# Kernel tuning notes

Measured on AMD Instinct MI355X. Metric: run time of the kernel, lower is better.

## Reference

```python
import jax, jax.numpy as jnp
import numpy as np

B, S, HID = 2, 2048, 2048
H = 16
HD = HID // H            # 128
HD2 = HD // 2            # 64 (rope dim per head)
LAT = HID // 8           # 256 latent dim
BASE = 10000.0


def _rotary_table(seq_len):
    # inv_freq over rope dim HD2
    inv_freq = 1.0 / (BASE ** (jnp.arange(0, HD2, 2, dtype=jnp.float32) / HD2))  # [HD2//2]
    pos = jnp.arange(seq_len, dtype=jnp.float32)
    sincos = pos[:, None] * inv_freq[None, :]                 # [S, HD2//2]
    return jnp.concatenate([jnp.sin(sincos), jnp.cos(sincos)], axis=-1)  # [S, HD2]


def _apply_rope(x, emb):
    # x: [B, S, H, HD2]; emb: [S, HD2]
    half = HD2 // 2
    x1, x2 = x[..., :half], x[..., half:]
    sin = emb[None, :, None, :half]
    cos = emb[None, :, None, half:]
    return jnp.concatenate([x1 * cos - x2 * sin, x1 * sin + x2 * cos], axis=-1)


def setup_inputs() -> dict:
    key = jax.random.key(0)
    ks = jax.random.split(key, 9)
    s = 0.02
    return {
        "hidden_states": jax.random.normal(ks[0], (B, S, HID), jnp.float32),
        "w_kv_d": jax.random.normal(ks[1], (HID, LAT), jnp.float32) * s,
        "w_q_d": jax.random.normal(ks[2], (HID, LAT), jnp.float32) * s,
        "w_k_u": jax.random.normal(ks[3], (LAT, H * HD2), jnp.float32) * s,
        "w_q_u": jax.random.normal(ks[4], (LAT, H * HD2), jnp.float32) * s,
        "w_v_u": jax.random.normal(ks[5], (LAT, H * HD), jnp.float32) * s,
        "w_rope_k": jax.random.normal(ks[6], (HID, HID // 2), jnp.float32) * s,
        "w_rope_q": jax.random.normal(ks[7], (LAT, HID // 2), jnp.float32) * s,
        "w_o": jax.random.normal(ks[8], (HID, HID), jnp.float32) * s,
    }


def reference(hidden_states, w_kv_d, w_q_d, w_k_u, w_q_u, w_v_u, w_rope_k, w_rope_q, w_o):
    b, s, _ = hidden_states.shape
    kv_d = hidden_states @ w_kv_d            # [B,S,LAT]
    q_d = hidden_states @ w_q_d              # [B,S,LAT]
    k_p = (kv_d @ w_k_u).reshape(b, s, H, HD2)
    q_p = (q_d @ w_q_u).reshape(b, s, H, HD2)
    v = (kv_d @ w_v_u).reshape(b, s, H, HD)
    k_r = (hidden_states @ w_rope_k).reshape(b, s, H, HD2)
    q_r = (q_d @ w_rope_q).reshape(b, s, H, HD2)

    emb = _rotary_table(s)
    k_r = _apply_rope(k_r, emb)
    q_r = _apply_rope(q_r, emb)

    k = jnp.concatenate([k_p, k_r], axis=-1)  # [B,S,H,HD]
    q = jnp.concatenate([q_p, q_r], axis=-1)

    scores = jnp.einsum('bqhd,bkhd->bhqk', q, k) / jnp.sqrt(jnp.float32(HD))
    causal = jnp.tril(jnp.ones((s, s), dtype=bool))
    scores = jnp.where(causal[None, None], scores, jnp.float32(-1e9))
    probs = jax.nn.softmax(scores, axis=-1)
    out = jnp.einsum('bhqk,bkhd->bqhd', probs, v).reshape(b, s, HID)
    return out @ w_o
```

## Files before the change

kernel.cpp:

```cpp
#include <hip/hip_runtime.h>
#include <hip/hip_bf16.h>

#define BB 2
#define SS 2048
#define HID 2048
#define NH 16
#define BS (BB*SS)
#define SCALE 0.088388347648318447f
#define C2LOG 0.12751743f

typedef __bf16 bf16x8 __attribute__((ext_vector_type(8)));
typedef float f32x4 __attribute__((ext_vector_type(4)));
typedef float f32x16 __attribute__((ext_vector_type(16)));
typedef unsigned int uintx2 __attribute__((ext_vector_type(2)));

__device__ __forceinline__ bf16x8 ld_frag(const __hip_bfloat16* p) {
    uint4 u = *reinterpret_cast<const uint4*>(p);
    return __builtin_bit_cast(bf16x8, u);
}
__device__ __forceinline__ unsigned int cvt_pk_bf16(float a, float b) {
    unsigned int r;
    asm("v_cvt_pk_bf16_f32 %0, %1, %2" : "=v"(r) : "v"(a), "v"(b));
    return r;
}
__device__ __forceinline__ ushort bf_bits(float v) {
    return (ushort)cvt_pk_bf16(v, v);
}
__device__ __forceinline__ void store_c(__hip_bfloat16* C, size_t idx, float v) {
    *reinterpret_cast<ushort*>(&C[idx]) = bf_bits(v);
}
__device__ __forceinline__ void store_c(float* C, size_t idx, float v) {
    C[idx] = v;
}

#define GLD16(gp, lp) \
  __builtin_amdgcn_global_load_lds((const __attribute__((address_space(1))) void*)(gp), \
                                   (__attribute__((address_space(3))) void*)(lp), 16, 0, 0)


__global__ __launch_bounds__(256) void convert_kernel(
    const float* __restrict__ src, __hip_bfloat16* __restrict__ dst, int n8)
{
    int i = blockIdx.x * blockDim.x + threadIdx.x;
    if (i >= n8) return;
    float4 a = reinterpret_cast<const float4*>(src)[2 * i];
    float4 b = reinterpret_cast<const float4*>(src)[2 * i + 1];
    uint4 o;
    o.x = cvt_pk_bf16(a.x, a.y);
    o.y = cvt_pk_bf16(a.z, a.w);
    o.z = cvt_pk_bf16(b.x, b.y);
    o.w = cvt_pk_bf16(b.z, b.w);
    reinterpret_cast<uint4*>(dst)[i] = o;
}

__global__ __launch_bounds__(256) void transpose_weights_kernel(
    const float* s0, const float* s1, const float* s2, const float* s3,
    const float* s4, const float* s5, const float* s6, const float* s7,
    __hip_bfloat16* WT1, __hip_bfloat16* WT2, __hip_bfloat16* WT3,
    __hip_bfloat16* WTo)
{
    const float* srcs[8] = { s0, s1, s2, s3, s4, s5, s6, s7 };
    const int Rs[8] = { 2048, 2048, 2048, 256, 256, 256, 256, 2048 };
    const int Cs[8] = { 256, 256, 1024, 1024, 2048, 1024, 1024, 2048 };
    __hip_bfloat16* dsts[8] = {
        WT1, WT1 + (size_t)256 * 2048, WT1 + (size_t)512 * 2048,
        WT2, WT2 + (size_t)1024 * 256,
        WT3, WT3 + (size_t)1024 * 256,
        WTo };
    const int prefix[9] = { 0, 512, 1024, 3072, 3328, 3840, 4096, 4352, 8448 };

    int bid = blockIdx.x;
    int seg = 0;
    #pragma unroll
    for (int i = 0; i < 8; i++) if (bid >= prefix[i + 1]) seg = i + 1;
    int local = bid - prefix[seg];
    int R = Rs[seg], C = Cs[seg];
    int tilesC = C / 32;
    int tr = local / tilesC, tc = local % tilesC;
    int r0 = tr * 32, c0 = tc * 32;
    const float* src = srcs[seg];
    __hip_bfloat16* dst = dsts[seg];

    __shared__ float Ts[32][33];
    int t = threadIdx.x;
    int ty = t >> 5, tx = t & 31;
    #pragma unroll
    for (int k = 0; k < 4; k++) {
        int r = ty + k * 8;
        Ts[r][tx] = src[(size_t)(r0 + r) * C + c0 + tx];
    }
    __syncthreads();
    #pragma unroll
    for (int k = 0; k < 4; k++) {
        int r = ty + k * 8;
        *reinterpret_cast<ushort*>(&dst[(size_t)(c0 + r) * R + r0 + tx]) =
            bf_bits(Ts[tx][r]);
    }
}

template <typename TC>
__global__ __launch_bounds__(256) void gemm_bt_kernel(
    const __hip_bfloat16* __restrict__ A, int lda,
    const __hip_bfloat16* __restrict__ Bt,
    TC* __restrict__ C0, int ldc0, int sp0, int off0, float cm0,
    TC* __restrict__ C1, int ldc1, int sp1, int off1, float cm1,
    int splitN, int K)
{
    __shared__ alignas(16) __hip_bfloat16 As[128 * 32];
    __shared__ alignas(16) __hip_bfloat16 Bs[128 * 32];

    const int nwg = gridDim.x * gridDim.y;
    int lin = blockIdx.y * gridDim.x + blockIdx.x;
    lin = (lin & 7) * (nwg >> 3) + (lin >> 3);
    const int bn = (lin % gridDim.x) * 128;
    const int bm = (lin / gridDim.x) * 128;

    const int t = threadIdx.x;
    const int w = t >> 6;
    const int lane = t & 63;
    const int l15 = lane & 15;
    const int quad = lane >> 4;
    const int wm = (w & 1) * 64;
    const int wn = (w >> 1) * 64;

    const int srow = lane >> 2;
    const int skcol = (lane & 3) * 8;

    f32x4 acc[4][4] = {};

    for (int k0 = 0; k0 < K; k0 += 32) {
        __syncthreads();
        #pragma unroll
        for (int i = 0; i < 2; i++) {
            int r = w * 32 + i * 16 + srow;
            GLD16(A + (size_t)(bm + r) * lda + k0 + skcol, &As[r * 32 + skcol]);
            GLD16(Bt + (size_t)(bn + r) * K + k0 + skcol, &Bs[r * 32 + skcol]);
        }
        __syncthreads();

        bf16x8 af[4], bf[4];
        #pragma unroll
        for (int mt = 0; mt < 4; mt++)
            af[mt] = ld_frag(&As[(wm + mt * 16 + l15) * 32 + quad * 8]);
        #pragma unroll
        for (int nt = 0; nt < 4; nt++)
            bf[nt] = ld_frag(&Bs[(wn + nt * 16 + l15) * 32 + quad * 8]);
        #pragma unroll
        for (int mt = 0; mt < 4; mt++)
            #pragma unroll
            for (int nt = 0; nt < 4; nt++)
                acc[mt][nt] = __builtin_amdgcn_mfma_f32_16x16x32_bf16(
                    af[mt], bf[nt], acc[mt][nt], 0, 0, 0);
    }

    #pragma unroll
    for (int nt = 0; nt < 4; nt++) {
        int col = bn + wn + nt * 16 + l15;
        TC* Cp; int c, ld, s64, off; float cm;
        if (col < splitN) { Cp = C0; c = col; ld = ldc0; s64 = sp0; off = off0; cm = cm0; }
        else { Cp = C1; c = col - splitN; ld = ldc1; s64 = sp1; off = off1; cm = cm1; }
        if (s64 == 2) {
            #pragma unroll
            for (int mt = 0; mt < 4; mt++) {
                int row0 = bm + wm + mt * 16 + quad * 4;
                #pragma unroll
                for (int r = 0; r < 4; r++)
                    store_c(Cp, (size_t)c * 4096 + row0 + r, acc[mt][nt][r] * cm);
            }
        } else if (s64 == 3) {
            const int hh = c >> 6, d = off + (c & 63);
            const size_t dbase = (size_t)(d >> 4) * 512
                               + (size_t)((d >> 3) & 1) * 256 + (d & 7);
            #pragma unroll
            for (int mt = 0; mt < 4; mt++) {
                #pragma unroll
                for (int r = 0; r < 4; r++) {
                    int m = bm + wm + mt * 16 + quad * 4 + r;
                    int bb2 = m >> 11, kv = m & 2047;
                    size_t idx = (size_t)(bb2 * 16 + hh) * 262144
                               + (size_t)(kv >> 5) * 4096 + dbase
                               + (size_t)(kv & 31) * 8;
                    store_c(Cp, idx, acc[mt][nt][r] * cm);
                }
            }
        } else if (s64 == 4) {
            const int hh = c >> 7, d = c & 127;
            const size_t dbase = (size_t)(d >> 5) * 2048 + (size_t)(d & 31) * 8;
            #pragma unroll
            for (int mt = 0; mt < 4; mt++) {
                #pragma unroll
                for (int r = 0; r < 4; r++) {
                    int m = bm + wm + mt * 16 + quad * 4 + r;
                    int bb2 = m >> 11, kv = m & 2047;
                    size_t idx = (size_t)(bb2 * 16 + hh) * 262144
                               + (size_t)(kv >> 6) * 8192 + dbase
                               + (size_t)((kv >> 4) & 3) * 512
                               + (size_t)((kv >> 3) & 1) * 256 + (kv & 7);
                    store_c(Cp, idx, acc[mt][nt][r] * cm);
                }
            }
        } else {
            int oc = s64 ? ((c >> 6) * 128 + (c & 63) + off) : c;
            #pragma unroll
            for (int mt = 0; mt < 4; mt++) {
                #pragma unroll
                for (int r = 0; r < 4; r++) {
                    int row = bm + wm + mt * 16 + quad * 4 + r;
                    store_c(Cp, (size_t)row * ld + oc, acc[mt][nt][r] * cm);
                }
            }
        }
    }
}

__global__ __launch_bounds__(256) void rope_kernel(
    __hip_bfloat16* __restrict__ Kf, __hip_bfloat16* __restrict__ Qb)
{
    int idx = blockIdx.x * blockDim.x + threadIdx.x;
    if (idx >= BS * NH * 32) return;
    int i = idx & 31;
    int h = (idx >> 5) & 15;
    int row = idx >> 9;
    int s = row & (SS - 1);
    int b = row >> 11;

    float inv = exp2f(-(float)i * 0.4152410118609203f);
    float ang = (float)s * inv;
    float sn = sinf(ang), cs = cosf(ang);

    {
        size_t kaddr = ((size_t)(b * 16 + h) * 64 + (s >> 5)) * 4096
                     + (size_t)(4 + (i >> 4)) * 512
                     + (size_t)(((i >> 3) & 1) * 32 + (s & 31)) * 8 + (i & 7);
        float x1 = __bfloat162float(Kf[kaddr]);
        float x2 = __bfloat162float(Kf[kaddr + 1024]);
        *reinterpret_cast<ushort*>(&Kf[kaddr])        = bf_bits(x1 * cs - x2 * sn);
        *reinterpret_cast<ushort*>(&Kf[kaddr + 1024]) = bf_bits(x1 * sn + x2 * cs);
    }
    {
        size_t obase = (size_t)row * 2048 + h * 128 + 64 + i;
        float x1 = __bfloat162float(Qb[obase]);
        float x2 = __bfloat162float(Qb[obase + 32]);
        *reinterpret_cast<ushort*>(&Qb[obase])      = bf_bits(x1 * cs - x2 * sn);
        *reinterpret_cast<ushort*>(&Qb[obase + 32]) = bf_bits(x1 * sn + x2 * cs);
    }
}

__global__ __launch_bounds__(512) void flash_attn_kernel(
    const __hip_bfloat16* __restrict__ Q,
    const __hip_bfloat16* __restrict__ Kf,
    const __hip_bfloat16* __restrict__ Vf,
    __hip_bfloat16* __restrict__ O)
{
    __shared__ alignas(16) __hip_bfloat16 Ktd[2 * 16 * 512];
    __shared__ alignas(16) __hip_bfloat16 Vsd[2 * 16 * 512];

    const int p = blockIdx.y & 7;
    const int h = blockIdx.x + 8 * (blockIdx.y >> 3);
    const int b = blockIdx.z;
    const int t = threadIdx.x;
    const int w = t >> 6;
    const int lane = t & 63;
    const int l31 = lane & 31;
    const int hi = lane >> 5;

    const int qt = (w < 4) ? (15 - p) : p;
    const int wq = w & 3;
    const int qwb = qt * 128 + wq * 32;
    const int q = qwb + l31;
    const int my_nt = 2 * qt + 1 + (wq >> 1);
    const int nbig = 2 * (15 - p) + 2;

    const __hip_bfloat16* Kfb = Kf + (size_t)(b * 16 + h) * 262144;
    const __hip_bfloat16* Vfb = Vf + (size_t)(b * 16 + h) * 262144;

    bf16x8 qf[8];
    {
        const __hip_bfloat16* qrow = Q + (size_t)(b * SS + q) * 2048 + h * 128;
        #pragma unroll
        for (int s = 0; s < 8; s++)
            qf[s] = ld_frag(qrow + s * 16 + hi * 8);
    }

    const int kreg = (w & 1) * 8 + (w >> 1) * 2;
    const int loff = lane * 8;
    const __hip_bfloat16* kp = Kfb + (size_t)((w & 1) * 4096 + (w >> 1) * 1024) + loff;
    const __hip_bfloat16* vp = Vfb + (size_t)(2 * w) * 512 + loff;
    __hip_bfloat16* kd[2] = { &Ktd[kreg * 512 + loff], &Ktd[8192 + kreg * 512 + loff] };
    __hip_bfloat16* vd[2] = { &Vsd[2 * w * 512 + loff], &Vsd[8192 + 2 * w * 512 + loff] };

    float m_i = -INFINITY;
    float l_i = 0.0f;
    f32x16 acc[4] = {};

    GLD16(kp, kd[0]);
    GLD16(kp + 512, kd[0] + 512);
    GLD16(vp, vd[0]);
    GLD16(vp + 512, vd[0] + 512);
    kp += 8192; vp += 8192;
    asm volatile("" :: "v"(qf[0]), "v"(qf[1]), "v"(qf[2]), "v"(qf[3]),
                       "v"(qf[4]), "v"(qf[5]), "v"(qf[6]), "v"(qf[7]));

    for (int kt = 0; kt < nbig; kt++) {
        const int kvb = kt * 64;
        const int par = kt & 1;
        const bool active = (kt < my_nt);

        asm volatile("s_waitcnt vmcnt(0)" ::: "memory");
        __builtin_amdgcn_s_barrier();
        asm volatile("" ::: "memory");

        {
            const int pn = par ^ 1;
            GLD16(kp, kd[pn]);
            GLD16(kp + 512, kd[pn] + 512);
            GLD16(vp, vd[pn]);
            GLD16(vp + 512, vd[pn] + 512);
            if (kt + 2 < nbig) { kp += 8192; vp += 8192; }
        }

        if (active) {
            const __hip_bfloat16* kb_base = &Ktd[par * 8192];
            const __hip_bfloat16* vb_base = &Vsd[par * 8192];

            f32x16 st[2] = {};
            __builtin_amdgcn_s_setprio(1);
            #pragma unroll
            for (int s = 0; s < 8; s++)
                #pragma unroll
                for (int kb = 0; kb < 2; kb++) {
                    bf16x8 kf = ld_frag(kb_base + (kb * 8 + s) * 512 + loff);
                    st[kb] = __builtin_amdgcn_mfma_f32_32x32x16_bf16(
                        kf, qf[s], st[kb], 0, 0, 0);
                }
            __builtin_amdgcn_s_setprio(0);

            float tmx;
            if (kvb + 63 > qwb) {
                const int thr = q - kvb - 4 * hi;
                tmx = -INFINITY;
                #pragma unroll
                for (int kb = 0; kb < 2; kb++)
                    #pragma unroll
                    for (int g = 0; g < 4; g++)
                        #pragma unroll
                        for (int r = 0; r < 4; r++) {
                            const int e = g * 4 + r;
                            float v = (kb * 32 + 8 * g + r <= thr) ? st[kb][e] : -INFINITY;
                            st[kb][e] = v;
                            tmx = fmaxf(tmx, v);
                        }
            } else {
                tmx = fmaxf(st[0][0], st[0][1]);
                #pragma unroll
                for (int e = 2; e < 16; e += 2)
                    tmx = fmaxf(fmaxf(tmx, st[0][e]), st[0][e + 1]);
                #pragma unroll
                for (int e = 0; e < 16; e += 2)
                    tmx = fmaxf(fmaxf(tmx, st[1][e]), st[1][e + 1]);
            }
            tmx = fmaxf(tmx, __shfl_xor(tmx, 32));
            const float m2x = tmx * C2LOG;

            const bool nosc = __all(m2x <= m_i + 8.0f);
            const float mnew = nosc ? m_i : fmaxf(m_i, m2x);
            float rs = 0.0f;
            #pragma unroll
            for (int kb = 0; kb < 2; kb++)
                #pragma unroll
                for (int e = 0; e < 16; e++) {
                    float pv = exp2f(fmaf(st[kb][e], C2LOG, -mnew));
                    st[kb][e] = pv;
                    rs += pv;
                }
            rs += __shfl_xor(rs, 32);
            if (!nosc) {
                const float alpha = exp2f(m_i - mnew);
                m_i = mnew;
                l_i *= alpha;
                #pragma unroll
                for (int dt = 0; dt < 4; dt++)
                    #pragma unroll
                    for (int e = 0; e < 16; e++)
                        acc[dt][e] *= alpha;
            }
            l_i += rs;

            uint4 af[4];
            #pragma unroll
            for (int kb = 0; kb < 2; kb++) {
                unsigned int pk[4][2];
                #pragma unroll
                for (int g = 0; g < 4; g++)
                    #pragma unroll
                    for (int i = 0; i < 2; i++)
                        pk[g][i] = cvt_pk_bf16(st[kb][g * 4 + 2 * i],
                                               st[kb][g * 4 + 2 * i + 1]);
                #pragma unroll
                for (int sl = 0; sl < 2; sl++) {
                    uintx2 r0 = __builtin_amdgcn_permlane32_swap(
                        pk[2 * sl][0], pk[2 * sl + 1][0], false, false);
                    uintx2 r1 = __builtin_amdgcn_permlane32_swap(
                        pk[2 * sl][1], pk[2 * sl + 1][1], false, false);
                    af[kb * 2 + sl] = make_uint4(r0[0], r1[0], r0[1], r1[1]);
                }
            }

            __builtin_amdgcn_s_setprio(1);
            #pragma unroll
            for (int s = 0; s < 4; s++) {
                bf16x8 pf = __builtin_bit_cast(bf16x8, af[s]);
                #pragma unroll
                for (int dt = 0; dt < 4; dt++) {
                    bf16x8 vf = ld_frag(vb_base + (dt * 4 + s) * 512 + loff);
                    acc[dt] = __builtin_amdgcn_mfma_f32_32x32x16_bf16(
                        vf, pf, acc[dt], 0, 0, 0);
                }
            }
            __builtin_amdgcn_s_setprio(0);
        }
    }

    const float inv_l = 1.0f / l_i;
    __hip_bfloat16* orow = O + (size_t)(b * SS + q) * 2048 + h * 128;
    #pragma unroll
    for (int dt = 0; dt < 4; dt++)
        #pragma unroll
        for (int g = 0; g < 4; g++) {
            uint2 uu;
            uu.x = cvt_pk_bf16(acc[dt][g * 4 + 0] * inv_l, acc[dt][g * 4 + 1] * inv_l);
            uu.y = cvt_pk_bf16(acc[dt][g * 4 + 2] * inv_l, acc[dt][g * 4 + 3] * inv_l);
            *reinterpret_cast<uint2*>(orow + dt * 32 + 8 * g + 4 * hi) = uu;
        }
}

extern "C" void kernel_launch(void* const* d_in, const int* in_sizes, int n_in,
                              void* d_out, int out_size, void* d_ws, size_t ws_size,
                              hipStream_t stream)
{
    const float* hs       = (const float*)d_in[0];
    const float* w_kv_d   = (const float*)d_in[1];
    const float* w_q_d    = (const float*)d_in[2];
    const float* w_k_u    = (const float*)d_in[3];
    const float* w_q_u    = (const float*)d_in[4];
    const float* w_v_u    = (const float*)d_in[5];
    const float* w_rope_k = (const float*)d_in[6];
    const float* w_rope_q = (const float*)d_in[7];
    const float* w_o      = (const float*)d_in[8];
    float* out = (float*)d_out;

    char* p = (char*)d_ws;
    auto alloc = [&](size_t nelem) {
        __hip_bfloat16* r = (__hip_bfloat16*)p;
        p += nelem * sizeof(__hip_bfloat16);
        return r;
    };
    __hip_bfloat16* hsb  = alloc((size_t)BS * HID);
    __hip_bfloat16* qkvd = alloc((size_t)BS * 512);
    __hip_bfloat16* WT1  = alloc((size_t)1536 * 2048);
    __hip_bfloat16* WT2  = alloc((size_t)3072 * 256);
    __hip_bfloat16* WT3  = alloc((size_t)2048 * 256);
    __hip_bfloat16* WTo  = alloc((size_t)2048 * 2048);
    __hip_bfloat16* Kf   = alloc((size_t)BS * HID);
    __hip_bfloat16* Qbuf = alloc((size_t)BS * HID);
    __hip_bfloat16* Vf   = alloc((size_t)HID * BS);
    __hip_bfloat16* attn = hsb;

    dim3 blk(256);

    convert_kernel<<<dim3((BS * HID / 8 + 255) / 256), blk, 0, stream>>>(
        hs, hsb, BS * HID / 8);
    transpose_weights_kernel<<<dim3(8448), blk, 0, stream>>>(
        w_kv_d, w_q_d, w_rope_k, w_k_u, w_v_u, w_q_u, w_rope_q, w_o,
        WT1, WT2, WT3, WTo);

    gemm_bt_kernel<__hip_bfloat16><<<dim3(1536 / 128, BS / 128), blk, 0, stream>>>(
        hsb, 2048, WT1,
        qkvd, 512, 0, 0, 1.0f,
        Kf, 0, 3, 64, 1.0f,
        512, 2048);
    gemm_bt_kernel<__hip_bfloat16><<<dim3(3072 / 128, BS / 128), blk, 0, stream>>>(
        qkvd, 512, WT2,
        Kf, 0, 3, 0, 1.0f,
        Vf, 0, 4, 0, 1.0f,
        1024, 256);
    gemm_bt_kernel<__hip_bfloat16><<<dim3(2048 / 128, BS / 128), blk, 0, stream>>>(
        qkvd + 256, 512, WT3,
        Qbuf, 2048, 1, 0, 1.0f,
        Qbuf, 2048, 1, 64, 1.0f,
        1024, 256);
    rope_kernel<<<dim3((BS * NH * 32 + 255) / 256), blk, 0, stream>>>(Kf, Qbuf);
    flash_attn_kernel<<<dim3(8, NH, BB), dim3(512), 0, stream>>>(
        Qbuf, Kf, Vf, attn);
    gemm_bt_kernel<float><<<dim3(2048 / 128, BS / 128), blk, 0, stream>>>(
        attn, 2048, WTo,
        out, 2048, 0, 0, 1.0f,
        out, 2048, 0, 0, 1.0f,
        2048, 2048);
}
```

Before: 334.5 us.

## Load K/V fragments directly from global memory, dropping LDS double-buffering

Removes the shared-memory double-buffered K/V staging and per-tile block barriers in the flash attention kernel. Each wave now loads its K and V MFMA fragments straight from global (pre-swizzled) memory into registers and iterates only over its own causal tile count. This removes barriers and lets waves with fewer tiles exit early. The cost is redundant global/L2 traffic across the 8 waves and exposed load latency, since there is no software prefetch.

```diff
diff --git a/kernel.cpp b/kernel.cpp
--- a/kernel.cpp
+++ b/kernel.cpp
@@ -252,9 +252,6 @@
     const __hip_bfloat16* __restrict__ Vf,
     __hip_bfloat16* __restrict__ O)
 {
-    __shared__ alignas(16) __hip_bfloat16 Ktd[2 * 16 * 512];
-    __shared__ alignas(16) __hip_bfloat16 Vsd[2 * 16 * 512];
-
     const int p = blockIdx.y & 7;
     const int h = blockIdx.x + 8 * (blockIdx.y >> 3);
     const int b = blockIdx.z;
@@ -269,7 +266,6 @@
     const int qwb = qt * 128 + wq * 32;
     const int q = qwb + l31;
     const int my_nt = 2 * qt + 1 + (wq >> 1);
-    const int nbig = 2 * (15 - p) + 2;
 
     const __hip_bfloat16* Kfb = Kf + (size_t)(b * 16 + h) * 262144;
     const __hip_bfloat16* Vfb = Vf + (size_t)(b * 16 + h) * 262144;
@@ -282,143 +278,124 @@
             qf[s] = ld_frag(qrow + s * 16 + hi * 8);
     }
 
-    const int kreg = (w & 1) * 8 + (w >> 1) * 2;
     const int loff = lane * 8;
-    const __hip_bfloat16* kp = Kfb + (size_t)((w & 1) * 4096 + (w >> 1) * 1024) + loff;
-    const __hip_bfloat16* vp = Vfb + (size_t)(2 * w) * 512 + loff;
-    __hip_bfloat16* kd[2] = { &Ktd[kreg * 512 + loff], &Ktd[8192 + kreg * 512 + loff] };
-    __hip_bfloat16* vd[2] = { &Vsd[2 * w * 512 + loff], &Vsd[8192 + 2 * w * 512 + loff] };
+    const __hip_bfloat16* kptr = Kfb + loff;
+    const __hip_bfloat16* vptr = Vfb + loff;
 
     float m_i = -INFINITY;
     float l_i = 0.0f;
     f32x16 acc[4] = {};
 
-    GLD16(kp, kd[0]);
-    GLD16(kp + 512, kd[0] + 512);
-    GLD16(vp, vd[0]);
-    GLD16(vp + 512, vd[0] + 512);
-    kp += 8192; vp += 8192;
-    asm volatile("" :: "v"(qf[0]), "v"(qf[1]), "v"(qf[2]), "v"(qf[3]),
-                       "v"(qf[4]), "v"(qf[5]), "v"(qf[6]), "v"(qf[7]));
-
-    for (int kt = 0; kt < nbig; kt++) {
+    for (int kt = 0; kt < my_nt; kt++) {
         const int kvb = kt * 64;
-        const int par = kt & 1;
-        const bool active = (kt < my_nt);
-
-        asm volatile("s_waitcnt vmcnt(0)" ::: "memory");
-        __builtin_amdgcn_s_barrier();
-        asm volatile("" ::: "memory");
-
-        {
-            const int pn = par ^ 1;
-            GLD16(kp, kd[pn]);
-            GLD16(kp + 512, kd[pn] + 512);
-            GLD16(vp, vd[pn]);
-            GLD16(vp + 512, vd[pn] + 512);
-            if (kt + 2 < nbig) { kp += 8192; vp += 8192; }
-        }
-
-        if (active) {
-            const __hip_bfloat16* kb_base = &Ktd[par * 8192];
-            const __hip_bfloat16* vb_base = &Vsd[par * 8192];
-
-            f32x16 st[2] = {};
-            __builtin_amdgcn_s_setprio(1);
+
+        bf16x8 kfr[2][8];
+        #pragma unroll
+        for (int kb = 0; kb < 2; kb++)
             #pragma unroll
             for (int s = 0; s < 8; s++)
-                #pragma unroll
-                for (int kb = 0; kb < 2; kb++) {
-                    bf16x8 kf = ld_frag(kb_base + (kb * 8 + s) * 512 + loff);
-                    st[kb] = __builtin_amdgcn_mfma_f32_32x32x16_bf16(
-                        kf, qf[s], st[kb], 0, 0, 0);
-                }
-            __builtin_amdgcn_s_setprio(0);
-
-            float tmx;
-            if (kvb + 63 > qwb) {
-                const int thr = q - kvb - 4 * hi;
-                tmx = -INFINITY;
-                #pragma unroll
-                for (int kb = 0; kb < 2; kb++)
-                    #pragma unroll
-                    for (int g = 0; g < 4; g++)
-                        #pragma unroll
-                        for (int r = 0; r < 4; r++) {
-                            const int e = g * 4 + r;
-                            float v = (kb * 32 + 8 * g + r <= thr) ? st[kb][e] : -INFINITY;
-                            st[kb][e] = v;
-                            tmx = fmaxf(tmx, v);
-                        }
-            } else {
-                tmx = fmaxf(st[0][0], st[0][1]);
-                #pragma unroll
-                for (int e = 2; e < 16; e += 2)
-                    tmx = fmaxf(fmaxf(tmx, st[0][e]), st[0][e + 1]);
-                #pragma unroll
-                for (int e = 0; e < 16; e += 2)
-                    tmx = fmaxf(fmaxf(tmx, st[1][e]), st[1][e + 1]);
-            }
-            tmx = fmaxf(tmx, __shfl_xor(tmx, 32));
-            const float m2x = tmx * C2LOG;
-
-            const bool nosc = __all(m2x <= m_i + 8.0f);
-            const float mnew = nosc ? m_i : fmaxf(m_i, m2x);
-            float rs = 0.0f;
+                kfr[kb][s] = ld_frag(kptr + (kb * 8 + s) * 512);
+
+        f32x16 st[2] = {};
+        __builtin_amdgcn_s_setprio(1);
+        #pragma unroll
+        for (int s = 0; s < 8; s++)
             #pragma unroll
             for (int kb = 0; kb < 2; kb++)
-                #pragma unroll
-                for (int e = 0; e < 16; e++) {
-                    float pv = exp2f(fmaf(st[kb][e], C2LOG, -mnew));
-                    st[kb][e] = pv;
-                    rs += pv;
-                }
-            rs += __shfl_xor(rs, 32);
-            if (!nosc) {
-                const float alpha = exp2f(m_i - mnew);
-                m_i = mnew;
-                l_i *= alpha;
-                #pragma unroll
-                for (int dt = 0; dt < 4; dt++)
-                    #pragma unroll
-                    for (int e = 0; e < 16; e++)
-                        acc[dt][e] *= alpha;
-            }
-            l_i += rs;
-
-            uint4 af[4];
-            #pragma unroll
-            for (int kb = 0; kb < 2; kb++) {
-                unsigned int pk[4][2];
+                st[kb] = __builtin_amdgcn_mfma_f32_32x32x16_bf16(
+                    kfr[kb][s], qf[s], st[kb], 0, 0, 0);
+        __builtin_amdgcn_s_setprio(0);
+
+        bf16x8 vfr[4][4];
+        #pragma unroll
+        for (int dt = 0; dt < 4; dt++)
+            #pragma unroll
+            for (int s = 0; s < 4; s++)
+                vfr[dt][s] = ld_frag(vptr + (dt * 4 + s) * 512);
+
+        float tmx;
+        if (kvb + 63 > qwb) {
+            const int thr = q - kvb - 4 * hi;
+            tmx = -INFINITY;
+            #pragma unroll
+            for (int kb = 0; kb < 2; kb++)
                 #pragma unroll
                 for (int g = 0; g < 4; g++)
                     #pragma unroll
-                    for (int i = 0; i < 2; i++)
-                        pk[g][i] = cvt_pk_bf16(st[kb][g * 4 + 2 * i],
-                                               st[kb][g * 4 + 2 * i + 1]);
-                #pragma unroll
-                for (int sl = 0; sl < 2; sl++) {
-                    uintx2 r0 = __builtin_amdgcn_permlane32_swap(
-                        pk[2 * sl][0], pk[2 * sl + 1][0], false, false);
-                    uintx2 r1 = __builtin_amdgcn_permlane32_swap(
-                        pk[2 * sl][1], pk[2 * sl + 1][1], false, false);
-                    af[kb * 2 + sl] = make_uint4(r0[0], r1[0], r0[1], r1[1]);
-                }
-            }
-
-            __builtin_amdgcn_s_setprio(1);
-            #pragma unroll
-            for (int s = 0; s < 4; s++) {
-                bf16x8 pf = __builtin_bit_cast(bf16x8, af[s]);
-                #pragma unroll
-                for (int dt = 0; dt < 4; dt++) {
-                    bf16x8 vf = ld_frag(vb_base + (dt * 4 + s) * 512 + loff);
-                    acc[dt] = __builtin_amdgcn_mfma_f32_32x32x16_bf16(
-                        vf, pf, acc[dt], 0, 0, 0);
-                }
-            }
-            __builtin_amdgcn_s_setprio(0);
-        }
+                    for (int r = 0; r < 4; r++) {
+                        const int e = g * 4 + r;
+                        float v = (kb * 32 + 8 * g + r <= thr) ? st[kb][e] : -INFINITY;
+                        st[kb][e] = v;
+                        tmx = fmaxf(tmx, v);
+                    }
+        } else {
+            tmx = fmaxf(st[0][0], st[0][1]);
+            #pragma unroll
+            for (int e = 2; e < 16; e += 2)
+                tmx = fmaxf(fmaxf(tmx, st[0][e]), st[0][e + 1]);
+            #pragma unroll
+            for (int e = 0; e < 16; e += 2)
+                tmx = fmaxf(fmaxf(tmx, st[1][e]), st[1][e + 1]);
+        }
+        tmx = fmaxf(tmx, __shfl_xor(tmx, 32));
+        const float m2x = tmx * C2LOG;
+
+        const bool nosc = __all(m2x <= m_i + 8.0f);
+        const float mnew = nosc ? m_i : fmaxf(m_i, m2x);
+        float rs = 0.0f;
+        #pragma unroll
+        for (int kb = 0; kb < 2; kb++)
+            #pragma unroll
+            for (int e = 0; e < 16; e++) {
+                float pv = exp2f(fmaf(st[kb][e], C2LOG, -mnew));
+                st[kb][e] = pv;
+                rs += pv;
+            }
+        rs += __shfl_xor(rs, 32);
+        if (!nosc) {
+            const float alpha = exp2f(m_i - mnew);
+            m_i = mnew;
+            l_i *= alpha;
+            #pragma unroll
+            for (int dt = 0; dt < 4; dt++)
+                #pragma unroll
+                for (int e = 0; e < 16; e++)
+                    acc[dt][e] *= alpha;
+        }
+        l_i += rs;
+
+        uint4 af[4];
+        #pragma unroll
+        for (int kb = 0; kb < 2; kb++) {
+            unsigned int pk[4][2];
+            #pragma unroll
+            for (int g = 0; g < 4; g++)
+                #pragma unroll
+                for (int i = 0; i < 2; i++)
+                    pk[g][i] = cvt_pk_bf16(st[kb][g * 4 + 2 * i],
+                                           st[kb][g * 4 + 2 * i + 1]);
+            #pragma unroll
+            for (int sl = 0; sl < 2; sl++) {
+                uintx2 r0 = __builtin_amdgcn_permlane32_swap(
+                    pk[2 * sl][0], pk[2 * sl + 1][0], false, false);
+                uintx2 r1 = __builtin_amdgcn_permlane32_swap(
+                    pk[2 * sl][1], pk[2 * sl + 1][1], false, false);
+                af[kb * 2 + sl] = make_uint4(r0[0], r1[0], r0[1], r1[1]);
+            }
+        }
+
+        __builtin_amdgcn_s_setprio(1);
+        #pragma unroll
+        for (int s = 0; s < 4; s++) {
+            bf16x8 pf = __builtin_bit_cast(bf16x8, af[s]);
+            #pragma unroll
+            for (int dt = 0; dt < 4; dt++)
+                acc[dt] = __builtin_amdgcn_mfma_f32_32x32x16_bf16(
+                    vfr[dt][s], pf, acc[dt], 0, 0, 0);
+        }
+        __builtin_amdgcn_s_setprio(0);
+
+        kptr += 8192; vptr += 8192;
     }
 
     const float inv_l = 1.0f / l_i;
```

Measured after the change: 330.3 us. About the same (-1.2%).
